# Kernel tuning notes

Hardware: AMD Instinct MI355X
Metric: run time of the kernel (lower is better)

The kernel has to match this reference:

```python
import jax, jax.numpy as jnp
import numpy as np
from jax import lax

EPS = 1e-5
MIN_SAMPLES = 4
RESHAPE = 14        # edge-map downsample factor
KEEP_FRAC = 0.1     # 1 - quantile(0.9)
KERNEL_FRAC = 0.05  # eval-mode log_kernel

SOBEL_X = jnp.array([[-1., 0., 1.], [-2., 0., 2.], [-1., 0., 1.]], jnp.float32)
SOBEL_Y = jnp.array([[-1., -2., -1.], [0., 0., 0.], [1., 2., 1.]], jnp.float32)


def _dwconv3(x, k):
    C = x.shape[1]
    kern = jnp.broadcast_to(k, (C, 1, 3, 3)).astype(x.dtype)
    return lax.conv_general_dilated(x, kern, (1, 1), 'SAME',
        feature_group_count=C, dimension_numbers=('NCHW', 'OIHW', 'NCHW'))


def _erode3(m):
    k = jnp.ones((1, 1, 3, 3), m.dtype)
    s = lax.conv_general_dilated(m, k, (1, 1), 'SAME',
        dimension_numbers=('NCHW', 'OIHW', 'NCHW'))
    return (s >= 9.0).astype(m.dtype)


def _masked_mean(x, mask, axis=-1):
    m = mask.astype(x.dtype)
    return jnp.sum(x * m, axis=axis) / jnp.maximum(jnp.sum(m, axis=axis), 1.0)


def _ssi_norm(x, mask):
    # scale-shift-invariant normalization: masked median shift, masked MAD scale
    big = jnp.where(mask, x, jnp.inf)
    srt = jnp.sort(big, axis=-1)
    n = jnp.sum(mask, axis=-1)
    idx = jnp.maximum((n - 1) // 2, 0)
    med = jnp.take_along_axis(srt, idx[..., None], axis=-1)
    med = jnp.where(n[..., None] > 0, med, 0.0)
    scale = _masked_mean(jnp.abs(x - med), mask, axis=-1)[..., None]
    return (x - med) / jnp.maximum(scale, EPS)


def _get_edge(image, vmask):
    gx = _dwconv3(image, SOBEL_X) / 8.0
    gy = _dwconv3(image, SOBEL_Y) / 8.0
    gx = jnp.sqrt(jnp.mean(gx * gx, axis=1, keepdims=True))
    gy = jnp.sqrt(jnp.mean(gy * gy, axis=1, keepdims=True))
    edges = jnp.sqrt(gx * gx + gy * gy)
    H, W = edges.shape[-2:]
    bm = jnp.zeros((H, W), edges.dtype).at[3:H - 3, 3:W - 3].set(1.0)
    return edges * bm * vmask


def _resize_bilinear(x, oh, ow):
    # torch F.interpolate bilinear, align_corners=False, no antialias
    B, C, H, W = x.shape
    def coords(o, s):
        c = jnp.clip((jnp.arange(o) + 0.5) * (s / o) - 0.5, 0.0, s - 1.0)
        i0 = jnp.floor(c).astype(jnp.int32)
        return i0, jnp.minimum(i0 + 1, s - 1), c - i0
    y0, y1, wy = coords(oh, H)
    x0, x1, wx = coords(ow, W)
    wy = wy[:, None]; wx = wx[None, :]
    g = lambda yi, xi: x[:, :, yi[:, None], xi[None, :]]
    return (g(y0, x0) * (1 - wy) * (1 - wx) + g(y0, x1) * (1 - wy) * wx
          + g(y1, x0) * wy * (1 - wx) + g(y1, x1) * wy * wx)


def _sample_edges(edges):
    B, _, H, W = edges.shape
    oh, ow = H // RESHAPE, W // RESHAPE
    e = _resize_bilinear(edges, oh, ow).reshape(B, -1)
    k = max(int(KEEP_FRAC * oh * ow), 10)
    _, idx = lax.top_k(e, k)
    return jnp.stack([(idx // ow) * RESHAPE, (idx % ow) * RESHAPE], -1).astype(jnp.int32)


def _extract_patches(x, coords, kh, kw):
    # vectorized irregular patch gather: [B,C,H,W] + [B,P,2] -> [B,P*C,kh*kw]
    B, C, H, W = x.shape
    ph, pw = kh // 2, kw // 2
    xp = jnp.pad(x, ((0, 0), (0, 0), (ph, ph), (pw, pw)))
    dy = jnp.arange(-ph, ph + 1)
    dx = jnp.arange(-pw, pw + 1)
    def one(img, y, x_):
        return img[:, (y + dy)[:, None], (x_ + dx)[None, :]]
    patches = jax.vmap(jax.vmap(one, in_axes=(None, 0, 0)))(
        xp, coords[..., 0] + ph, coords[..., 1] + pw)  # [B,P,C,kh,kw]
    return patches.reshape(B, -1, kh * kw)


def _forward(inp, tgt, mask, image, vmask):
    mask = mask.astype(bool)
    inp = inp.astype(jnp.float32)
    tgt = tgt.astype(jnp.float32)
    B, _, H, W = inp.shape
    vm = _erode3(vmask.astype(jnp.float32))
    edges = _get_edge(image.astype(jnp.float32), vm)
    coords = _sample_edges(edges)
    ks = int(KERNEL_FRAC * min(H, W))
    ks += int(ks % 2 == 0)
    # local patch branch
    pin = _extract_patches(inp, coords, ks, ks)
    ptg = _extract_patches(tgt, coords, ks, ks)
    pmk = _extract_patches(mask.astype(jnp.float32), coords, ks, ks) > 0.5
    pin = _ssi_norm(pin, pmk)
    ptg = _ssi_norm(ptg, pmk)
    err = jnp.maximum(jnp.abs(pin - ptg), EPS)
    valid = jnp.sum(pmk, axis=-1) >= MIN_SAMPLES
    ep = jnp.sqrt(jnp.maximum(_masked_mean(err, pmk, -1), EPS))  # [B,P]
    e_patch = _masked_mean(ep, valid, -1)                         # [B]
    # global image branch
    gi = _ssi_norm(inp.reshape(B, 1, H * W), mask.reshape(B, 1, H * W))
    gt = _ssi_norm(tgt.reshape(B, 1, H * W), mask.reshape(B, 1, H * W))
    gerr = jnp.maximum(jnp.abs(gi - gt), EPS)
    e_glob = jnp.sqrt(jnp.maximum(_masked_mean(gerr, mask.reshape(B, 1, H * W), -1), EPS)).squeeze(-1)
    return 0.5 * (e_patch + e_glob)  # [B]


def setup_inputs() -> dict:
    key = jax.random.key(0)
    k1, k2, k3, k4 = jax.random.split(key, 4)
    B, H, W = 32, 480, 640
    return {
        'input': jax.random.uniform(k1, (B, 1, H, W), jnp.float32, 0.1, 10.0),
        'target': jax.random.uniform(k2, (B, 1, H, W), jnp.float32, 0.1, 10.0),
        'mask': jax.random.bernoulli(k3, 0.9, (B, 1, H, W)),
        'image': jax.random.normal(k4, (B, 3, H, W), jnp.float32),
        'validity_mask': jnp.ones((B, 1, H, W), bool),
    }


def reference(input, target, mask, image, validity_mask):
    return _forward(input, target, mask, image, validity_mask)
```

## Files before the change

### kernel.cpp

```cpp
#include <hip/hip_runtime.h>
#include <math.h>

#define BB 32
#define HH 480
#define WW 640
#define HWN (HH * WW)
#define OH 34
#define OW 45
#define OHW (OH * OW)
#define KTOP 153
#define KS 25
#define PHW 12
#define PATCH (KS * KS)
#define RESHAPE_I 14
#define EPSV 1e-5f

#define TSLICE 10
#define TSW (OHW / TSLICE)

#define PSLICE 32
#define NSLICE 16
#define CAP 16384
#define LCAP 2048
#define CPAD 32

__device__ __forceinline__ unsigned int fkey(float f) {
  unsigned int u = __float_as_uint(f);
  return (u & 0x80000000u) ? ~u : (u | 0x80000000u);
}
__device__ __forceinline__ float fkey_inv(unsigned int k) {
  unsigned int u = (k & 0x80000000u) ? (k & 0x7FFFFFFFu) : ~k;
  return __uint_as_float(u);
}

__device__ __forceinline__ float breduce256(float v, float* red) {
  const int t = threadIdx.x;
  __syncthreads();
  red[t] = v;
  __syncthreads();
  for (int s2 = 128; s2 > 0; s2 >>= 1) {
    if (t < s2) red[t] += red[t + s2];
    __syncthreads();
  }
  float r = red[0];
  __syncthreads();
  return r;
}

__device__ __forceinline__ float2 breduce256x2(float a, float b, float* red) {
  const int t = threadIdx.x;
  __syncthreads();
  red[t] = a;
  red[256 + t] = b;
  __syncthreads();
  for (int s2 = 128; s2 > 0; s2 >>= 1) {
    if (t < s2) {
      red[t] += red[t + s2];
      red[256 + t] += red[256 + t + s2];
    }
    __syncthreads();
  }
  float2 r = make_float2(red[0], red[256]);
  __syncthreads();
  return r;
}

__device__ float edge_at(const float* __restrict__ image, const unsigned char* __restrict__ vmask,
                         int b, int y, int x) {
  if (y < 3 || y >= HH - 3 || x < 3 || x >= WW - 3) return 0.f;
  const unsigned char* vm = vmask + (size_t)b * HWN;
  #pragma unroll
  for (int dy = -1; dy <= 1; ++dy) {
    #pragma unroll
    for (int dx = -1; dx <= 1; ++dx) {
      if (!vm[(size_t)(y + dy) * WW + (x + dx)]) return 0.f;
    }
  }
  const float* img = image + (size_t)b * 3 * HWN;
  float sx2 = 0.f, sy2 = 0.f;
  #pragma unroll
  for (int c = 0; c < 3; ++c) {
    const float* p = img + (size_t)c * HWN + (size_t)y * WW + x;
    float a00 = p[-WW - 1], a01 = p[-WW], a02 = p[-WW + 1];
    float a10 = p[-1],                    a12 = p[1];
    float a20 = p[WW - 1],  a21 = p[WW],  a22 = p[WW + 1];
    float gx = (-a00 + a02 + -2.f * a10 + 2.f * a12 + -a20 + a22) / 8.f;
    float gy = (-a00 + -2.f * a01 + -a02 + a20 + 2.f * a21 + a22) / 8.f;
    sx2 += gx * gx;
    sy2 += gy * gy;
  }
  float gxm = sqrtf(sx2 / 3.f);
  float gym = sqrtf(sy2 / 3.f);
  return sqrtf(gxm * gxm + gym * gym);
}

__global__ __launch_bounds__(256) void edge_resize_kernel(const float* __restrict__ image,
                                                          const unsigned char* __restrict__ vmask,
                                                          float* __restrict__ re) {
  int gid = blockIdx.x * 256 + threadIdx.x;
  int corner = gid & 3;
  int cell = gid >> 2;
  int b = cell / OHW;
  int rem = cell % OHW;
  int oy = rem / OW, ox = rem % OW;

  const float ry = (float)((double)HH / (double)OH);
  const float rx = (float)((double)WW / (double)OW);
  float cy = fminf(fmaxf(((float)oy + 0.5f) * ry - 0.5f, 0.f), (float)(HH - 1));
  float cx = fminf(fmaxf(((float)ox + 0.5f) * rx - 0.5f, 0.f), (float)(WW - 1));
  int y0 = (int)floorf(cy);
  int x0 = (int)floorf(cx);
  int y1 = min(y0 + 1, HH - 1);
  int x1 = min(x0 + 1, WW - 1);
  float wy = cy - (float)y0;
  float wx = cx - (float)x0;

  int yy = (corner & 2) ? y1 : y0;
  int xx = (corner & 1) ? x1 : x0;
  float w = ((corner & 2) ? wy : 1.f - wy) * ((corner & 1) ? wx : 1.f - wx);
  float g = edge_at(image, vmask, b, yy, xx) * w;
  g += __shfl_xor(g, 1, 64);
  g += __shfl_xor(g, 2, 64);
  if (corner == 0) re[cell] = g;
}

__global__ __launch_bounds__(256) void topk_rank_kernel(const float* __restrict__ re,
                                                        int* __restrict__ rpart) {
  const int b = blockIdx.x / TSLICE;
  const int sl = blockIdx.x % TSLICE;
  const int t = threadIdx.x;
  __shared__ float e[OHW];
  for (int i = t; i < OHW; i += 256) e[i] = re[b * OHW + i];
  __syncthreads();

  float vi[6];
  int idx[6], cnt[6];
  #pragma unroll
  for (int q = 0; q < 6; ++q) {
    int i = t + q * 256;
    idx[q] = i;
    vi[q] = (i < OHW) ? e[i] : 0.f;
    cnt[q] = 0;
  }
  const int j0 = sl * TSW;
  for (int jj = 0; jj < TSW; ++jj) {
    int j = j0 + jj;
    float u = e[j];
    #pragma unroll
    for (int q = 0; q < 6; ++q) {
      cnt[q] += (u > vi[q]) || (u == vi[q] && j < idx[q]);
    }
  }
  int* rp = rpart + ((size_t)b * TSLICE + sl) * OHW;
  #pragma unroll
  for (int q = 0; q < 6; ++q) {
    if (idx[q] < OHW) rp[idx[q]] = cnt[q];
  }
}

__global__ __launch_bounds__(256) void topk_write_kernel(const int* __restrict__ rpart,
                                                         int* __restrict__ coords) {
  const int b = blockIdx.x;
  const int t = threadIdx.x;
  const int* rp = rpart + (size_t)b * TSLICE * OHW;
  for (int i = t; i < OHW; i += 256) {
    int rank = 0;
    #pragma unroll
    for (int sl = 0; sl < TSLICE; ++sl) rank += rp[sl * OHW + i];
    if (rank < KTOP) {
      coords[(b * KTOP + rank) * 2 + 0] = (i / OW) * RESHAPE_I;
      coords[(b * KTOP + rank) * 2 + 1] = (i % OW) * RESHAPE_I;
    }
  }
}

__global__ __launch_bounds__(64) void patch_kernel(const float* __restrict__ inp,
                                                   const float* __restrict__ tgt,
                                                   const unsigned char* __restrict__ mask,
                                                   const int* __restrict__ coords,
                                                   float* __restrict__ ep, float* __restrict__ val) {
  const int bk = blockIdx.x;
  const int b = bk / KTOP;
  const int t = threadIdx.x;
  __shared__ unsigned int hist[512];
  __shared__ unsigned int sh_pref[2];
  __shared__ int sh_rank[2];

  const int cy = coords[bk * 2 + 0];
  const int cx = coords[bk * 2 + 1];

  float v_in[10], v_tg[10];
  unsigned int k_in[10], k_tg[10];
  unsigned int mbits = 0;
  #pragma unroll
  for (int q = 0; q < 10; ++q) {
    int i = t + q * 64;
    float vi = 0.f, vt = 0.f;
    if (i < PATCH) {
      int dy = i / KS - PHW, dx = i % KS - PHW;
      int y = cy + dy, x = cx + dx;
      if (y >= 0 && y < HH && x >= 0 && x < WW) {
        size_t off = (size_t)b * HWN + (size_t)y * WW + x;
        if (mask[off]) mbits |= (1u << q);
        vi = inp[off];
        vt = tgt[off];
      }
    }
    v_in[q] = vi; v_tg[q] = vt;
    k_in[q] = fkey(vi); k_tg[q] = fkey(vt);
  }

  int pn = __popc(mbits);
  #pragma unroll
  for (int d = 32; d > 0; d >>= 1) pn += __shfl_xor(pn, d, 64);
  const int n = pn;
  const float nf = (float)n;
  const int r = (n > 0) ? ((n - 1) >> 1) : 0;

  if (t == 0) {
    sh_pref[0] = 0; sh_pref[1] = 0;
    sh_rank[0] = r; sh_rank[1] = r;
  }
  __syncthreads();

  #pragma unroll
  for (int p = 0; p < 4; ++p) {
    const int shift = 24 - 8 * p;
    #pragma unroll
    for (int j = 0; j < 8; ++j) hist[t + 64 * j] = 0;
    __syncthreads();
    const int r_in = sh_rank[0], r_tg = sh_rank[1];
    const unsigned int pref_in = sh_pref[0], pref_tg = sh_pref[1];
    #pragma unroll
    for (int q = 0; q < 10; ++q) {
      if (mbits & (1u << q)) {
        unsigned int k = k_in[q];
        if (p == 0 || (k >> (shift + 8)) == pref_in)
          atomicAdd(&hist[(k >> shift) & 255u], 1u);
        unsigned int k2 = k_tg[q];
        if (p == 0 || (k2 >> (shift + 8)) == pref_tg)
          atomicAdd(&hist[256 + ((k2 >> shift) & 255u)], 1u);
      }
    }
    __syncthreads();
    {
      unsigned int a0 = hist[t * 4 + 0], a1 = hist[t * 4 + 1];
      unsigned int a2 = hist[t * 4 + 2], a3 = hist[t * 4 + 3];
      unsigned int b0 = hist[256 + t * 4 + 0], b1 = hist[256 + t * 4 + 1];
      unsigned int b2 = hist[256 + t * 4 + 2], b3 = hist[256 + t * 4 + 3];
      unsigned int sa0 = a0, sa1 = sa0 + a1, sa2 = sa1 + a2, sa3 = sa2 + a3;
      unsigned int sb0 = b0, sb1 = sb0 + b1, sb2 = sb1 + b2, sb3 = sb2 + b3;
      unsigned int ta = sa3, tb = sb3;
      #pragma unroll
      for (int d = 1; d < 64; d <<= 1) {
        unsigned int ua = (unsigned int)__shfl_up((int)ta, d, 64);
        unsigned int ub = (unsigned int)__shfl_up((int)tb, d, 64);
        if (t >= d) { ta += ua; tb += ub; }
      }
      unsigned int exa = ta - sa3, exb = tb - sb3;
      unsigned int rra = (unsigned int)r_in, rrb = (unsigned int)r_tg;
      unsigned int pa[4] = {exa, exa + sa0, exa + sa1, exa + sa2};
      unsigned int ca[4] = {exa + sa0, exa + sa1, exa + sa2, exa + sa3};
      unsigned int pb[4] = {exb, exb + sb0, exb + sb1, exb + sb2};
      unsigned int cb[4] = {exb + sb0, exb + sb1, exb + sb2, exb + sb3};
      #pragma unroll
      for (int j = 0; j < 4; ++j) {
        if (rra >= pa[j] && rra < ca[j]) {
          sh_pref[0] = (pref_in << 8) | (unsigned int)(t * 4 + j);
          sh_rank[0] = (int)(rra - pa[j]);
        }
        if (rrb >= pb[j] && rrb < cb[j]) {
          sh_pref[1] = (pref_tg << 8) | (unsigned int)(t * 4 + j);
          sh_rank[1] = (int)(rrb - pb[j]);
        }
      }
    }
    __syncthreads();
  }

  const float med_i = (n > 0) ? fkey_inv(sh_pref[0]) : 0.f;
  const float med_t = (n > 0) ? fkey_inv(sh_pref[1]) : 0.f;

  float pi = 0.f, pt = 0.f;
  #pragma unroll
  for (int q = 0; q < 10; ++q) {
    if (mbits & (1u << q)) {
      pi += fabsf(v_in[q] - med_i);
      pt += fabsf(v_tg[q] - med_t);
    }
  }
  #pragma unroll
  for (int d = 32; d > 0; d >>= 1) {
    pi += __shfl_xor(pi, d, 64);
    pt += __shfl_xor(pt, d, 64);
  }
  const float si = fmaxf(pi / fmaxf(nf, 1.f), EPSV);
  const float st = fmaxf(pt / fmaxf(nf, 1.f), EPSV);

  float pe = 0.f;
  #pragma unroll
  for (int q = 0; q < 10; ++q) {
    if (mbits & (1u << q)) {
      float a = (v_in[q] - med_i) / si;
      float c = (v_tg[q] - med_t) / st;
      pe += fmaxf(fabsf(a - c), EPSV);
    }
  }
  #pragma unroll
  for (int d = 32; d > 0; d >>= 1) pe += __shfl_xor(pe, d, 64);

  if (t == 0) {
    ep[bk] = sqrtf(fmaxf(pe / fmaxf(nf, 1.f), EPSV));
    val[bk] = (n >= 4) ? 1.f : 0.f;
  }
}

__global__ __launch_bounds__(256) void preduce_kernel(const float* __restrict__ ep,
                                                      const float* __restrict__ val,
                                                      float* __restrict__ e_patch) {
  const int b = blockIdx.x;
  const int t = threadIdx.x;
  __shared__ float red[512];
  float se = 0.f, sv = 0.f;
  for (int i = t; i < KTOP; i += 256) {
    float v = val[b * KTOP + i];
    se += ep[b * KTOP + i] * v;
    sv += v;
  }
  float2 tt = breduce256x2(se, sv, red);
  if (t == 0) e_patch[b] = tt.x / fmaxf(tt.y, 1.f);
}

__global__ __launch_bounds__(256) void gpassA_kernel(const float* __restrict__ inp,
                                                     const float* __restrict__ tgt,
                                                     const unsigned char* __restrict__ mask,
                                                     unsigned int* __restrict__ ghistA) {
  const int b = blockIdx.x / PSLICE;
  const int sl = blockIdx.x % PSLICE;
  const int t = threadIdx.x;
  __shared__ unsigned int hist[512];
  hist[t] = 0; hist[t + 256] = 0;
  __syncthreads();
  const float4* xi4 = (const float4*)(inp + (size_t)b * HWN);
  const float4* xt4 = (const float4*)(tgt + (size_t)b * HWN);
  const unsigned int* m4 = (const unsigned int*)(mask + (size_t)b * HWN);
  const int per4 = (HWN / PSLICE) / 4;
  const int s0 = sl * per4;
  for (int i = s0 + t; i < s0 + per4; i += 256) {
    unsigned int mm = m4[i];
    if (!mm) continue;
    float4 a = xi4[i], c = xt4[i];
    if (mm & 0x000000FFu) { atomicAdd(&hist[fkey(a.x) >> 24], 1u); atomicAdd(&hist[256 + (fkey(c.x) >> 24)], 1u); }
    if (mm & 0x0000FF00u) { atomicAdd(&hist[fkey(a.y) >> 24], 1u); atomicAdd(&hist[256 + (fkey(c.y) >> 24)], 1u); }
    if (mm & 0x00FF0000u) { atomicAdd(&hist[fkey(a.z) >> 24], 1u); atomicAdd(&hist[256 + (fkey(c.z) >> 24)], 1u); }
    if (mm & 0xFF000000u) { atomicAdd(&hist[fkey(a.w) >> 24], 1u); atomicAdd(&hist[256 + (fkey(c.w) >> 24)], 1u); }
  }
  __syncthreads();
  unsigned int h0 = hist[t], h1 = hist[t + 256];
  if (h0) atomicAdd(&ghistA[(b * 2 + 0) * 256 + t], h0);
  if (h1) atomicAdd(&ghistA[(b * 2 + 1) * 256 + t], h1);
}

__global__ __launch_bounds__(64) void gselA_kernel(const unsigned int* __restrict__ ghistA,
                                                   int* __restrict__ selA) {
  const int bs = blockIdx.x;
  if (threadIdx.x != 0) return;
  const unsigned int* gh = ghistA + bs * 256;
  unsigned int n = 0;
  for (int i = 0; i < 256; ++i) n += gh[i];
  int c1 = -1, r1 = 0;
  unsigned int nb = 0;
  if (n > 0) {
    unsigned int r = (n - 1) >> 1, cum = 0;
    int bin = 0;
    for (; bin < 256; ++bin) {
      unsigned int h = gh[bin];
      if (cum + h > r) break;
      cum += h;
    }
    c1 = bin; r1 = (int)(r - cum); nb = cum;
  }
  selA[bs * 4 + 0] = c1;
  selA[bs * 4 + 1] = r1;
  selA[bs * 4 + 2] = (int)n;
  selA[bs * 4 + 3] = (int)nb;
}

__global__ __launch_bounds__(256) void gpassB_kernel(const float* __restrict__ inp,
                                                     const float* __restrict__ tgt,
                                                     const unsigned char* __restrict__ mask,
                                                     const int* __restrict__ selA,
                                                     unsigned int* __restrict__ ghistB) {
  const int b = blockIdx.x / PSLICE;
  const int sl = blockIdx.x % PSLICE;
  const int t = threadIdx.x;
  __shared__ unsigned int hist[512];
  hist[t] = 0; hist[t + 256] = 0;
  __syncthreads();
  const unsigned int c1i = (unsigned int)selA[(b * 2 + 0) * 4];
  const unsigned int c1t = (unsigned int)selA[(b * 2 + 1) * 4];
  const float4* xi4 = (const float4*)(inp + (size_t)b * HWN);
  const float4* xt4 = (const float4*)(tgt + (size_t)b * HWN);
  const unsigned int* m4 = (const unsigned int*)(mask + (size_t)b * HWN);
  const int per4 = (HWN / PSLICE) / 4;
  const int s0 = sl * per4;
  for (int i = s0 + t; i < s0 + per4; i += 256) {
    unsigned int mm = m4[i];
    if (!mm) continue;
    float4 a = xi4[i], c = xt4[i];
    #define GPB(av, cv, bit) \
      if (mm & bit) { \
        unsigned int k = fkey(av); \
        if ((k >> 24) == c1i) atomicAdd(&hist[(k >> 16) & 255u], 1u); \
        unsigned int k2 = fkey(cv); \
        if ((k2 >> 24) == c1t) atomicAdd(&hist[256 + ((k2 >> 16) & 255u)], 1u); \
      }
    GPB(a.x, c.x, 0x000000FFu)
    GPB(a.y, c.y, 0x0000FF00u)
    GPB(a.z, c.z, 0x00FF0000u)
    GPB(a.w, c.w, 0xFF000000u)
    #undef GPB
  }
  __syncthreads();
  unsigned int h0 = hist[t], h1 = hist[t + 256];
  if (h0) atomicAdd(&ghistB[(b * 2 + 0) * 256 + t], h0);
  if (h1) atomicAdd(&ghistB[(b * 2 + 1) * 256 + t], h1);
}

__global__ __launch_bounds__(64) void gselB_kernel(const unsigned int* __restrict__ ghistB,
                                                   const int* __restrict__ selA,
                                                   int* __restrict__ selB) {
  const int bs = blockIdx.x;
  if (threadIdx.x != 0) return;
  const int c1 = selA[bs * 4 + 0];
  const int r1 = selA[bs * 4 + 1];
  const int n = selA[bs * 4 + 2];
  const int nb1 = selA[bs * 4 + 3];
  if (c1 < 0) {
    selB[bs * 4 + 0] = -1;
    selB[bs * 4 + 1] = 0;
    selB[bs * 4 + 2] = 0;
    selB[bs * 4 + 3] = 0;
    return;
  }
  const unsigned int* gh = ghistB + bs * 256;
  unsigned int r = (unsigned int)r1, cum = 0;
  int bin = 0;
  for (; bin < 256; ++bin) {
    unsigned int h = gh[bin];
    if (cum + h > r) break;
    cum += h;
  }
  selB[bs * 4 + 0] = (c1 << 8) | bin;
  selB[bs * 4 + 1] = (int)(r - cum);
  selB[bs * 4 + 2] = n;
  selB[bs * 4 + 3] = nb1 + (int)cum;
}

__global__ __launch_bounds__(256) void gcollect_kernel(const float* __restrict__ inp,
                                                       const float* __restrict__ tgt,
                                                       const unsigned char* __restrict__ mask,
                                                       const int* __restrict__ selB,
                                                       float* __restrict__ cand,
                                                       unsigned int* __restrict__ ccount,
                                                       float* __restrict__ sbelow,
                                                       float* __restrict__ sabove) {
  const int bs = blockIdx.x / NSLICE;
  const int sl = blockIdx.x % NSLICE;
  const int b = bs >> 1, s = bs & 1;
  const float* x = (s == 0 ? inp : tgt) + (size_t)b * HWN;
  const unsigned char* m = mask + (size_t)b * HWN;
  const int prefix = selB[bs * 4 + 0];
  __shared__ float red[512];
  __shared__ float buf[LCAP];
  __shared__ unsigned int lcnt, gbase;
  const int t = threadIdx.x;
  if (t == 0) lcnt = 0;
  __syncthreads();
  float sb = 0.f, sa = 0.f;
  if (prefix >= 0) {
    float* cd = cand + (size_t)bs * CAP;
    const float4* x4 = (const float4*)x;
    const unsigned int* m4 = (const unsigned int*)m;
    const int per4 = (HWN / NSLICE) / 4;
    const int s0 = sl * per4;
    for (int i = s0 + t; i < s0 + per4; i += 256) {
      unsigned int mm = m4[i];
      if (!mm) continue;
      float4 a = x4[i];
      #define GCOL(av, bit) \
        if (mm & bit) { \
          float v = av; \
          int pf = (int)(fkey(v) >> 16); \
          if (pf < prefix) sb += v; \
          else if (pf > prefix) sa += v; \
          else { \
            unsigned int pos = atomicAdd(&lcnt, 1u); \
            if (pos < LCAP) buf[pos] = v; \
            else { \
              unsigned int g = atomicAdd(&ccount[bs * CPAD], 1u); \
              if (g < CAP) cd[g] = v; \
            } \
          } \
        }
      GCOL(a.x, 0x000000FFu)
      GCOL(a.y, 0x0000FF00u)
      GCOL(a.z, 0x00FF0000u)
      GCOL(a.w, 0xFF000000u)
      #undef GCOL
    }
  }
  __syncthreads();
  if (prefix >= 0) {
    unsigned int c = min(lcnt, (unsigned int)LCAP);
    if (t == 0 && c > 0) gbase = atomicAdd(&ccount[bs * CPAD], c);
    __syncthreads();
    if (c > 0) {
      float* cd = cand + (size_t)bs * CAP;
      unsigned int base = gbase;
      for (unsigned int i = t; i < c; i += 256) {
        unsigned int pos = base + i;
        if (pos < CAP) cd[pos] = buf[i];
      }
    }
  }
  float2 ts = breduce256x2(sb, sa, red);
  if (t == 0) {
    atomicAdd(&sbelow[bs], ts.x);
    atomicAdd(&sabove[bs], ts.y);
  }
}

__global__ __launch_bounds__(256) void gfinal_kernel(const float* __restrict__ cand,
                                                     const unsigned int* __restrict__ ccount,
                                                     const int* __restrict__ selB,
                                                     const float* __restrict__ sbelow,
                                                     const float* __restrict__ sabove,
                                                     float* __restrict__ gstats,
                                                     float* __restrict__ nvals) {
  const int bs = blockIdx.x;
  const int t = threadIdx.x;
  const int prefix = selB[bs * 4 + 0];
  const int r2 = selB[bs * 4 + 1];
  const int n = selB[bs * 4 + 2];
  const int nbelow = selB[bs * 4 + 3];
  __shared__ unsigned int hist[256];
  __shared__ float red[256];
  __shared__ int sh_bin1, sh_r3;
  const float* cd = cand + (size_t)bs * CAP;
  int c = (int)min(ccount[bs * CPAD], (unsigned int)CAP);
  if (prefix < 0) {
    if (t == 0) {
      gstats[bs * 2 + 0] = 0.f;
      gstats[bs * 2 + 1] = 0.f;
      if ((bs & 1) == 0) nvals[bs >> 1] = 0.f;
    }
    return;
  }

  hist[t] = 0;
  __syncthreads();
  for (int i = t; i < c; i += 256)
    atomicAdd(&hist[(fkey(cd[i]) >> 8) & 255u], 1u);
  __syncthreads();
  if (t == 0) {
    unsigned int rr = (unsigned int)r2, cum = 0;
    int bin = 0;
    for (; bin < 256; ++bin) {
      unsigned int h = hist[bin];
      if (cum + h > rr) break;
      cum += h;
    }
    sh_bin1 = bin;
    sh_r3 = (int)(rr - cum);
  }
  __syncthreads();
  const int bin1 = sh_bin1;
  const int r3 = sh_r3;

  hist[t] = 0;
  __syncthreads();
  for (int i = t; i < c; i += 256) {
    unsigned int key = fkey(cd[i]);
    if (((key >> 8) & 255u) == (unsigned int)bin1)
      atomicAdd(&hist[key & 255u], 1u);
  }
  __syncthreads();
  __shared__ float sh_med;
  if (t == 0) {
    unsigned int rr = (unsigned int)r3, cum = 0;
    int bin = 0;
    for (; bin < 256; ++bin) {
      unsigned int h = hist[bin];
      if (cum + h > rr) break;
      cum += h;
    }
    unsigned int key = ((unsigned int)prefix << 16) |
                       ((unsigned int)bin1 << 8) | (unsigned int)bin;
    sh_med = fkey_inv(key);
  }
  __syncthreads();
  const float med = sh_med;

  float ps = 0.f;
  for (int i = t; i < c; i += 256) ps += fabsf(cd[i] - med);
  float scand = breduce256(ps, red);
  if (t == 0) {
    float nb = (float)nbelow;
    float na = (float)(n - nbelow - c);
    float num = (nb * med - sbelow[bs]) + (sabove[bs] - na * med) + scand;
    gstats[bs * 2 + 0] = med;
    gstats[bs * 2 + 1] = num / fmaxf((float)n, 1.f);
    if ((bs & 1) == 0) nvals[bs >> 1] = (float)n;
  }
}

__global__ __launch_bounds__(256) void gerr_kernel(const float* __restrict__ inp,
                                                   const float* __restrict__ tgt,
                                                   const unsigned char* __restrict__ mask,
                                                   const float* __restrict__ gstats,
                                                   float* __restrict__ gacc) {
  const int b = blockIdx.x / PSLICE;
  const int sl = blockIdx.x % PSLICE;
  __shared__ float red[256];
  const int t = threadIdx.x;
  const float med_i = gstats[(b * 2 + 0) * 2 + 0];
  const float sc_i = fmaxf(gstats[(b * 2 + 0) * 2 + 1], EPSV);
  const float med_t = gstats[(b * 2 + 1) * 2 + 0];
  const float sc_t = fmaxf(gstats[(b * 2 + 1) * 2 + 1], EPSV);
  const float ri = 1.f / sc_i, rt = 1.f / sc_t;
  const float4* xi4 = (const float4*)(inp + (size_t)b * HWN);
  const float4* xt4 = (const float4*)(tgt + (size_t)b * HWN);
  const unsigned int* m4 = (const unsigned int*)(mask + (size_t)b * HWN);
  const int per4 = (HWN / PSLICE) / 4;
  const int s0 = sl * per4;
  float part = 0.f;
  for (int i = s0 + t; i < s0 + per4; i += 256) {
    unsigned int mm = m4[i];
    if (!mm) continue;
    float4 a = xi4[i], c = xt4[i];
    if (mm & 0x000000FFu) part += fmaxf(fabsf((a.x - med_i) * ri - (c.x - med_t) * rt), EPSV);
    if (mm & 0x0000FF00u) part += fmaxf(fabsf((a.y - med_i) * ri - (c.y - med_t) * rt), EPSV);
    if (mm & 0x00FF0000u) part += fmaxf(fabsf((a.z - med_i) * ri - (c.z - med_t) * rt), EPSV);
    if (mm & 0xFF000000u) part += fmaxf(fabsf((a.w - med_i) * ri - (c.w - med_t) * rt), EPSV);
  }
  float tp = breduce256(part, red);
  if (t == 0) atomicAdd(&gacc[b], tp);
}

__global__ __launch_bounds__(64) void final_kernel(const float* __restrict__ gacc,
                                                   const float* __restrict__ nvals,
                                                   const float* __restrict__ e_patch,
                                                   float* __restrict__ out) {
  const int b = threadIdx.x;
  if (b < BB) {
    float n = nvals[b];
    float eg = sqrtf(fmaxf(gacc[b] / fmaxf(n, 1.f), EPSV));
    out[b] = 0.5f * (e_patch[b] + eg);
  }
}

extern "C" void kernel_launch(void* const* d_in, const int* in_sizes, int n_in,
                              void* d_out, int out_size, void* d_ws, size_t ws_size,
                              hipStream_t stream) {
  const float* inp = (const float*)d_in[0];
  const float* tgt = (const float*)d_in[1];
  const unsigned char* mask = (const unsigned char*)d_in[2];
  const float* image = (const float*)d_in[3];
  const unsigned char* vmask = (const unsigned char*)d_in[4];
  float* out = (float*)d_out;

  float* ws = (float*)d_ws;
  float* re = ws;
  int* coords = (int*)(ws + 48960);
  float* ep = ws + 48960 + 9792;
  float* val = ep + 4896;
  float* e_patch = val + 4896;
  float* gstats = e_patch + 32;
  float* nvals = gstats + 128;
  int* selA = (int*)(nvals + 32);
  int* selB = selA + 256;
  float* cand = (float*)(selB + 256);
  unsigned int* ghistA = (unsigned int*)(cand + (size_t)64 * CAP);
  unsigned int* ghistB = ghistA + 64 * 256;
  unsigned int* ccount = ghistB + 64 * 256;
  float* sbelow = (float*)(ccount + 64 * CPAD);
  float* sabove = sbelow + 64;
  float* gacc = sabove + 64;
  size_t zero_bytes = ((size_t)64 * 256 * 2 + 64 * CPAD + 64 + 64 + 32) * 4;
  hipMemsetAsync(ghistA, 0, zero_bytes, stream);

  int* rpart = (int*)cand;

  edge_resize_kernel<<<(BB * OHW * 4) / 256, 256, 0, stream>>>(image, vmask, re);
  topk_rank_kernel<<<BB * TSLICE, 256, 0, stream>>>(re, rpart);
  topk_write_kernel<<<BB, 256, 0, stream>>>(rpart, coords);
  patch_kernel<<<BB * KTOP, 64, 0, stream>>>(inp, tgt, mask, coords, ep, val);
  preduce_kernel<<<BB, 256, 0, stream>>>(ep, val, e_patch);
  gpassA_kernel<<<BB * PSLICE, 256, 0, stream>>>(inp, tgt, mask, ghistA);
  gselA_kernel<<<BB * 2, 64, 0, stream>>>(ghistA, selA);
  gpassB_kernel<<<BB * PSLICE, 256, 0, stream>>>(inp, tgt, mask, selA, ghistB);
  gselB_kernel<<<BB * 2, 64, 0, stream>>>(ghistB, selA, selB);
  gcollect_kernel<<<BB * 2 * NSLICE, 256, 0, stream>>>(inp, tgt, mask, selB, cand, ccount, sbelow, sabove);
  gfinal_kernel<<<BB * 2, 256, 0, stream>>>(cand, ccount, selB, sbelow, sabove, gstats, nvals);
  gerr_kernel<<<BB * PSLICE, 256, 0, stream>>>(inp, tgt, mask, gstats, gacc);
  final_kernel<<<1, 64, 0, stream>>>(gacc, nvals, e_patch, out);
}
```

Baseline: 427.3 us.

## Merge two radix histogram passes into one 12-bit pass for global median

Replaces the two 8-bit radix-select passes over the full input/target (pass A, select A, pass B, select B) with a single 4096-bin histogram pass and a parallel prefix-scan selection kernel. This removes one full read of inp, tgt and mask, plus two kernel launches. In exchange, the coarser 12-bit prefix leaves many more candidates for gcollect and gfinal, so CAP is doubled and gfinal gains a third refinement level over the remaining 20 bits. The 32 KB shared histogram per block may also lower occupancy and add global atomic traffic.

```diff
diff --git a/kernel.cpp b/kernel.cpp
--- a/kernel.cpp
+++ b/kernel.cpp
@@ -18,9 +18,10 @@
 #define TSLICE 10
 #define TSW (OHW / TSLICE)
 
+#define NB12 4096
 #define PSLICE 32
 #define NSLICE 16
-#define CAP 16384
+#define CAP 32768
 #define LCAP 2048
 #define CPAD 32
 
@@ -331,15 +332,15 @@
   if (t == 0) e_patch[b] = tt.x / fmaxf(tt.y, 1.f);
 }
 
-__global__ __launch_bounds__(256) void gpassA_kernel(const float* __restrict__ inp,
-                                                     const float* __restrict__ tgt,
-                                                     const unsigned char* __restrict__ mask,
-                                                     unsigned int* __restrict__ ghistA) {
+__global__ __launch_bounds__(256) void gpass12_kernel(const float* __restrict__ inp,
+                                                      const float* __restrict__ tgt,
+                                                      const unsigned char* __restrict__ mask,
+                                                      unsigned int* __restrict__ ghist) {
   const int b = blockIdx.x / PSLICE;
   const int sl = blockIdx.x % PSLICE;
   const int t = threadIdx.x;
-  __shared__ unsigned int hist[512];
-  hist[t] = 0; hist[t + 256] = 0;
+  __shared__ unsigned int hist[2 * NB12];
+  for (int i = t; i < 2 * NB12; i += 256) hist[i] = 0;
   __syncthreads();
   const float4* xi4 = (const float4*)(inp + (size_t)b * HWN);
   const float4* xt4 = (const float4*)(tgt + (size_t)b * HWN);
@@ -350,117 +351,74 @@
     unsigned int mm = m4[i];
     if (!mm) continue;
     float4 a = xi4[i], c = xt4[i];
-    if (mm & 0x000000FFu) { atomicAdd(&hist[fkey(a.x) >> 24], 1u); atomicAdd(&hist[256 + (fkey(c.x) >> 24)], 1u); }
-    if (mm & 0x0000FF00u) { atomicAdd(&hist[fkey(a.y) >> 24], 1u); atomicAdd(&hist[256 + (fkey(c.y) >> 24)], 1u); }
-    if (mm & 0x00FF0000u) { atomicAdd(&hist[fkey(a.z) >> 24], 1u); atomicAdd(&hist[256 + (fkey(c.z) >> 24)], 1u); }
-    if (mm & 0xFF000000u) { atomicAdd(&hist[fkey(a.w) >> 24], 1u); atomicAdd(&hist[256 + (fkey(c.w) >> 24)], 1u); }
-  }
-  __syncthreads();
-  unsigned int h0 = hist[t], h1 = hist[t + 256];
-  if (h0) atomicAdd(&ghistA[(b * 2 + 0) * 256 + t], h0);
-  if (h1) atomicAdd(&ghistA[(b * 2 + 1) * 256 + t], h1);
-}
-
-__global__ __launch_bounds__(64) void gselA_kernel(const unsigned int* __restrict__ ghistA,
-                                                   int* __restrict__ selA) {
+    if (mm & 0x000000FFu) { atomicAdd(&hist[fkey(a.x) >> 20], 1u); atomicAdd(&hist[NB12 + (fkey(c.x) >> 20)], 1u); }
+    if (mm & 0x0000FF00u) { atomicAdd(&hist[fkey(a.y) >> 20], 1u); atomicAdd(&hist[NB12 + (fkey(c.y) >> 20)], 1u); }
+    if (mm & 0x00FF0000u) { atomicAdd(&hist[fkey(a.z) >> 20], 1u); atomicAdd(&hist[NB12 + (fkey(c.z) >> 20)], 1u); }
+    if (mm & 0xFF000000u) { atomicAdd(&hist[fkey(a.w) >> 20], 1u); atomicAdd(&hist[NB12 + (fkey(c.w) >> 20)], 1u); }
+  }
+  __syncthreads();
+  for (int i = t; i < NB12; i += 256) {
+    unsigned int h0 = hist[i], h1 = hist[NB12 + i];
+    if (h0) atomicAdd(&ghist[(size_t)(b * 2 + 0) * NB12 + i], h0);
+    if (h1) atomicAdd(&ghist[(size_t)(b * 2 + 1) * NB12 + i], h1);
+  }
+}
+
+__global__ __launch_bounds__(256) void gsel12_kernel(const unsigned int* __restrict__ ghist,
+                                                     int* __restrict__ sel) {
   const int bs = blockIdx.x;
-  if (threadIdx.x != 0) return;
-  const unsigned int* gh = ghistA + bs * 256;
-  unsigned int n = 0;
-  for (int i = 0; i < 256; ++i) n += gh[i];
-  int c1 = -1, r1 = 0;
-  unsigned int nb = 0;
-  if (n > 0) {
-    unsigned int r = (n - 1) >> 1, cum = 0;
-    int bin = 0;
-    for (; bin < 256; ++bin) {
-      unsigned int h = gh[bin];
-      if (cum + h > r) break;
+  const int t = threadIdx.x;
+  const unsigned int* gh = ghist + (size_t)bs * NB12;
+  __shared__ unsigned int scan[256];
+  unsigned int local[16];
+  unsigned int s = 0;
+  const int base = t * 16;
+  #pragma unroll
+  for (int j = 0; j < 16; ++j) {
+    local[j] = gh[base + j];
+    s += local[j];
+  }
+  scan[t] = s;
+  __syncthreads();
+  for (int d = 1; d < 256; d <<= 1) {
+    unsigned int v = (t >= d) ? scan[t - d] : 0u;
+    __syncthreads();
+    scan[t] += v;
+    __syncthreads();
+  }
+  const unsigned int incl = scan[t];
+  const unsigned int ex = incl - s;
+  const unsigned int n = scan[255];
+  if (n == 0) {
+    if (t == 0) {
+      sel[bs * 4 + 0] = -1;
+      sel[bs * 4 + 1] = 0;
+      sel[bs * 4 + 2] = 0;
+      sel[bs * 4 + 3] = 0;
+    }
+    return;
+  }
+  const unsigned int r = (n - 1) >> 1;
+  if (r >= ex && r < incl) {
+    unsigned int cum = ex;
+    int bin = base;
+    #pragma unroll
+    for (int j = 0; j < 16; ++j) {
+      unsigned int h = local[j];
+      if (cum + h > r) { bin = base + j; break; }
       cum += h;
     }
-    c1 = bin; r1 = (int)(r - cum); nb = cum;
-  }
-  selA[bs * 4 + 0] = c1;
-  selA[bs * 4 + 1] = r1;
-  selA[bs * 4 + 2] = (int)n;
-  selA[bs * 4 + 3] = (int)nb;
-}
-
-__global__ __launch_bounds__(256) void gpassB_kernel(const float* __restrict__ inp,
-                                                     const float* __restrict__ tgt,
-                                                     const unsigned char* __restrict__ mask,
-                                                     const int* __restrict__ selA,
-                                                     unsigned int* __restrict__ ghistB) {
-  const int b = blockIdx.x / PSLICE;
-  const int sl = blockIdx.x % PSLICE;
-  const int t = threadIdx.x;
-  __shared__ unsigned int hist[512];
-  hist[t] = 0; hist[t + 256] = 0;
-  __syncthreads();
-  const unsigned int c1i = (unsigned int)selA[(b * 2 + 0) * 4];
-  const unsigned int c1t = (unsigned int)selA[(b * 2 + 1) * 4];
-  const float4* xi4 = (const float4*)(inp + (size_t)b * HWN);
-  const float4* xt4 = (const float4*)(tgt + (size_t)b * HWN);
-  const unsigned int* m4 = (const unsigned int*)(mask + (size_t)b * HWN);
-  const int per4 = (HWN / PSLICE) / 4;
-  const int s0 = sl * per4;
-  for (int i = s0 + t; i < s0 + per4; i += 256) {
-    unsigned int mm = m4[i];
-    if (!mm) continue;
-    float4 a = xi4[i], c = xt4[i];
-    #define GPB(av, cv, bit) \
-      if (mm & bit) { \
-        unsigned int k = fkey(av); \
-        if ((k >> 24) == c1i) atomicAdd(&hist[(k >> 16) & 255u], 1u); \
-        unsigned int k2 = fkey(cv); \
-        if ((k2 >> 24) == c1t) atomicAdd(&hist[256 + ((k2 >> 16) & 255u)], 1u); \
-      }
-    GPB(a.x, c.x, 0x000000FFu)
-    GPB(a.y, c.y, 0x0000FF00u)
-    GPB(a.z, c.z, 0x00FF0000u)
-    GPB(a.w, c.w, 0xFF000000u)
-    #undef GPB
-  }
-  __syncthreads();
-  unsigned int h0 = hist[t], h1 = hist[t + 256];
-  if (h0) atomicAdd(&ghistB[(b * 2 + 0) * 256 + t], h0);
-  if (h1) atomicAdd(&ghistB[(b * 2 + 1) * 256 + t], h1);
-}
-
-__global__ __launch_bounds__(64) void gselB_kernel(const unsigned int* __restrict__ ghistB,
-                                                   const int* __restrict__ selA,
-                                                   int* __restrict__ selB) {
-  const int bs = blockIdx.x;
-  if (threadIdx.x != 0) return;
-  const int c1 = selA[bs * 4 + 0];
-  const int r1 = selA[bs * 4 + 1];
-  const int n = selA[bs * 4 + 2];
-  const int nb1 = selA[bs * 4 + 3];
-  if (c1 < 0) {
-    selB[bs * 4 + 0] = -1;
-    selB[bs * 4 + 1] = 0;
-    selB[bs * 4 + 2] = 0;
-    selB[bs * 4 + 3] = 0;
-    return;
-  }
-  const unsigned int* gh = ghistB + bs * 256;
-  unsigned int r = (unsigned int)r1, cum = 0;
-  int bin = 0;
-  for (; bin < 256; ++bin) {
-    unsigned int h = gh[bin];
-    if (cum + h > r) break;
-    cum += h;
-  }
-  selB[bs * 4 + 0] = (c1 << 8) | bin;
-  selB[bs * 4 + 1] = (int)(r - cum);
-  selB[bs * 4 + 2] = n;
-  selB[bs * 4 + 3] = nb1 + (int)cum;
+    sel[bs * 4 + 0] = bin;
+    sel[bs * 4 + 1] = (int)(r - cum);
+    sel[bs * 4 + 2] = (int)n;
+    sel[bs * 4 + 3] = (int)cum;
+  }
 }
 
 __global__ __launch_bounds__(256) void gcollect_kernel(const float* __restrict__ inp,
                                                        const float* __restrict__ tgt,
                                                        const unsigned char* __restrict__ mask,
-                                                       const int* __restrict__ selB,
+                                                       const int* __restrict__ sel,
                                                        float* __restrict__ cand,
                                                        unsigned int* __restrict__ ccount,
                                                        float* __restrict__ sbelow,
@@ -470,7 +428,7 @@
   const int b = bs >> 1, s = bs & 1;
   const float* x = (s == 0 ? inp : tgt) + (size_t)b * HWN;
   const unsigned char* m = mask + (size_t)b * HWN;
-  const int prefix = selB[bs * 4 + 0];
+  const int prefix = sel[bs * 4 + 0];
   __shared__ float red[512];
   __shared__ float buf[LCAP];
   __shared__ unsigned int lcnt, gbase;
@@ -491,7 +449,7 @@
       #define GCOL(av, bit) \
         if (mm & bit) { \
           float v = av; \
-          int pf = (int)(fkey(v) >> 16); \
+          int pf = (int)(fkey(v) >> 20); \
           if (pf < prefix) sb += v; \
           else if (pf > prefix) sa += v; \
           else { \
@@ -533,20 +491,20 @@
 
 __global__ __launch_bounds__(256) void gfinal_kernel(const float* __restrict__ cand,
                                                      const unsigned int* __restrict__ ccount,
-                                                     const int* __restrict__ selB,
+                                                     const int* __restrict__ sel,
                                                      const float* __restrict__ sbelow,
                                                      const float* __restrict__ sabove,
                                                      float* __restrict__ gstats,
                                                      float* __restrict__ nvals) {
   const int bs = blockIdx.x;
   const int t = threadIdx.x;
-  const int prefix = selB[bs * 4 + 0];
-  const int r2 = selB[bs * 4 + 1];
-  const int n = selB[bs * 4 + 2];
-  const int nbelow = selB[bs * 4 + 3];
+  const int prefix = sel[bs * 4 + 0];
+  const int r2 = sel[bs * 4 + 1];
+  const int n = sel[bs * 4 + 2];
+  const int nbelow = sel[bs * 4 + 3];
   __shared__ unsigned int hist[256];
   __shared__ float red[256];
-  __shared__ int sh_bin1, sh_r3;
+  __shared__ int sh_bin, sh_r;
   const float* cd = cand + (size_t)bs * CAP;
   int c = (int)min(ccount[bs * CPAD], (unsigned int)CAP);
   if (prefix < 0) {
@@ -561,7 +519,7 @@
   hist[t] = 0;
   __syncthreads();
   for (int i = t; i < c; i += 256)
-    atomicAdd(&hist[(fkey(cd[i]) >> 8) & 255u], 1u);
+    atomicAdd(&hist[(fkey(cd[i]) >> 12) & 255u], 1u);
   __syncthreads();
   if (t == 0) {
     unsigned int rr = (unsigned int)r2, cum = 0;
@@ -571,22 +529,21 @@
       if (cum + h > rr) break;
       cum += h;
     }
-    sh_bin1 = bin;
-    sh_r3 = (int)(rr - cum);
-  }
-  __syncthreads();
-  const int bin1 = sh_bin1;
-  const int r3 = sh_r3;
+    sh_bin = bin;
+    sh_r = (int)(rr - cum);
+  }
+  __syncthreads();
+  const int bin1 = sh_bin;
+  const int r3 = sh_r;
 
   hist[t] = 0;
   __syncthreads();
   for (int i = t; i < c; i += 256) {
-    unsigned int key = fkey(cd[i]);
-    if (((key >> 8) & 255u) == (unsigned int)bin1)
-      atomicAdd(&hist[key & 255u], 1u);
-  }
-  __syncthreads();
-  __shared__ float sh_med;
+    unsigned int k = fkey(cd[i]);
+    if (((k >> 12) & 255u) == (unsigned int)bin1)
+      atomicAdd(&hist[(k >> 4) & 255u], 1u);
+  }
+  __syncthreads();
   if (t == 0) {
     unsigned int rr = (unsigned int)r3, cum = 0;
     int bin = 0;
@@ -595,8 +552,36 @@
       if (cum + h > rr) break;
       cum += h;
     }
-    unsigned int key = ((unsigned int)prefix << 16) |
-                       ((unsigned int)bin1 << 8) | (unsigned int)bin;
+    sh_bin = bin;
+    sh_r = (int)(rr - cum);
+  }
+  __syncthreads();
+  const int bin2 = sh_bin;
+  const int r4 = sh_r;
+
+  if (t < 16) hist[t] = 0;
+  __syncthreads();
+  {
+    const unsigned int want = (((unsigned int)bin1 << 8) | (unsigned int)bin2);
+    for (int i = t; i < c; i += 256) {
+      unsigned int k = fkey(cd[i]);
+      if (((k >> 4) & 0xFFFFu) == want)
+        atomicAdd(&hist[k & 15u], 1u);
+    }
+  }
+  __syncthreads();
+  __shared__ float sh_med;
+  if (t == 0) {
+    unsigned int rr = (unsigned int)r4, cum = 0;
+    int bin = 0;
+    for (; bin < 16; ++bin) {
+      unsigned int h = hist[bin];
+      if (cum + h > rr) break;
+      cum += h;
+    }
+    unsigned int key = ((unsigned int)prefix << 20) |
+                       ((unsigned int)bin1 << 12) |
+                       ((unsigned int)bin2 << 4) | (unsigned int)bin;
     sh_med = fkey_inv(key);
   }
   __syncthreads();
@@ -678,17 +663,15 @@
   float* e_patch = val + 4896;
   float* gstats = e_patch + 32;
   float* nvals = gstats + 128;
-  int* selA = (int*)(nvals + 32);
-  int* selB = selA + 256;
-  float* cand = (float*)(selB + 256);
-  unsigned int* ghistA = (unsigned int*)(cand + (size_t)64 * CAP);
-  unsigned int* ghistB = ghistA + 64 * 256;
-  unsigned int* ccount = ghistB + 64 * 256;
+  int* sel12 = (int*)(nvals + 32);
+  float* cand = (float*)(sel12 + 256);
+  unsigned int* ghist12 = (unsigned int*)(cand + (size_t)64 * CAP);
+  unsigned int* ccount = ghist12 + (size_t)64 * NB12;
   float* sbelow = (float*)(ccount + 64 * CPAD);
   float* sabove = sbelow + 64;
   float* gacc = sabove + 64;
-  size_t zero_bytes = ((size_t)64 * 256 * 2 + 64 * CPAD + 64 + 64 + 32) * 4;
-  hipMemsetAsync(ghistA, 0, zero_bytes, stream);
+  size_t zero_bytes = ((size_t)64 * NB12 + 64 * CPAD + 64 + 64 + 32) * 4;
+  hipMemsetAsync(ghist12, 0, zero_bytes, stream);
 
   int* rpart = (int*)cand;
 
@@ -697,12 +680,10 @@
   topk_write_kernel<<<BB, 256, 0, stream>>>(rpart, coords);
   patch_kernel<<<BB * KTOP, 64, 0, stream>>>(inp, tgt, mask, coords, ep, val);
   preduce_kernel<<<BB, 256, 0, stream>>>(ep, val, e_patch);
-  gpassA_kernel<<<BB * PSLICE, 256, 0, stream>>>(inp, tgt, mask, ghistA);
-  gselA_kernel<<<BB * 2, 64, 0, stream>>>(ghistA, selA);
-  gpassB_kernel<<<BB * PSLICE, 256, 0, stream>>>(inp, tgt, mask, selA, ghistB);
-  gselB_kernel<<<BB * 2, 64, 0, stream>>>(ghistB, selA, selB);
-  gcollect_kernel<<<BB * 2 * NSLICE, 256, 0, stream>>>(inp, tgt, mask, selB, cand, ccount, sbelow, sabove);
-  gfinal_kernel<<<BB * 2, 256, 0, stream>>>(cand, ccount, selB, sbelow, sabove, gstats, nvals);
+  gpass12_kernel<<<BB * PSLICE, 256, 0, stream>>>(inp, tgt, mask, ghist12);
+  gsel12_kernel<<<BB * 2, 256, 0, stream>>>(ghist12, sel12);
+  gcollect_kernel<<<BB * 2 * NSLICE, 256, 0, stream>>>(inp, tgt, mask, sel12, cand, ccount, sbelow, sabove);
+  gfinal_kernel<<<BB * 2, 256, 0, stream>>>(cand, ccount, sel12, sbelow, sabove, gstats, nvals);
   gerr_kernel<<<BB * PSLICE, 256, 0, stream>>>(inp, tgt, mask, gstats, gacc);
   final_kernel<<<1, 64, 0, stream>>>(gacc, nvals, e_patch, out);
 }
```

Result: faster. 394.8 us (-7.6%).
